# Kernel optimization log

Measured on AMD Instinct MI355X. Metric: run time of the kernel, lower is better.

Reference implementation:

```python
import jax, jax.numpy as jnp
import numpy as np

N, T, J, NB = 2048, 81, 16, 15
D_ATT, HEADS, SEQ, D_LIN, NOISE = 48, 6, 31, 256, 45
BN_EPS, LN_EPS, SLOPE = 1e-5, 1e-6, 0.01

# Human3.6M 16-joint skeleton bone (parent, child) pairs
_BONES = [(0,1),(1,2),(2,3),(0,4),(4,5),(5,6),(0,7),(7,8),(8,9),(9,10),(8,11),(11,12),(12,13),(8,14),(14,15)]
BONES_P = np.array([p for p, c in _BONES])
BONES_C = np.array([c for p, c in _BONES])
_parent = {c: p for p, c in _BONES}
_bone_of = {c: i for i, (p, c) in enumerate(_BONES)}
_M = np.zeros((NB, J), np.float32)  # M[i,j]=1 iff bone i lies on root->joint j chain
for j in range(1, J):
    jj = j
    while jj != 0:
        _M[_bone_of[jj], j] = 1.0
        jj = _parent[jj]
M_BONE2POSE = jnp.asarray(_M)
FIXED_MASK = jnp.ones((NB,), jnp.float32).at[jnp.array([6, 7])].set(0.0)  # torso bones kept fixed


def _layer_norm(t, a, b):
    mean = t.mean(-1, keepdims=True)
    # torch.std default is unbiased (ddof=1); module divides by (std + eps)
    std = jnp.sqrt(((t - mean) ** 2).sum(-1, keepdims=True) / (t.shape[-1] - 1))
    return a * (t - mean) / (std + LN_EPS) + b


def _leaky(x):
    return jnp.where(x >= 0, x, SLOPE * x)


def _axis_angle_to_matrix(v):
    # Rodrigues: v (..., 3) axis-angle -> (..., 3, 3)
    theta = jnp.linalg.norm(v, axis=-1, keepdims=True)
    k = v / jnp.maximum(theta, 1e-8)
    c = jnp.cos(theta)[..., None]
    s = jnp.sin(theta)[..., None]
    kx, ky, kz = k[..., 0], k[..., 1], k[..., 2]
    z = jnp.zeros_like(kx)
    K = jnp.stack([jnp.stack([z, -kz, ky], -1),
                   jnp.stack([kz, z, -kx], -1),
                   jnp.stack([-ky, kx, z], -1)], -2)
    kk = k[..., :, None] * k[..., None, :]
    return c * jnp.eye(3, dtype=v.dtype) + s * K + (1 - c) * kk


def setup_inputs() -> dict:
    key = jax.random.key(0)
    ks = jax.random.split(key, 12)
    w = lambda k, shape, scale=0.05: jax.random.normal(k, shape, jnp.float32) * scale
    return {
        'inputs_3d': jax.random.normal(ks[0], (N, 1, T, J, 3), jnp.float32),
        'noise': jax.random.normal(ks[1], (N, NOISE), jnp.float32),
        'enc_w': w(ks[2], (D_ATT, 3)), 'enc_b': jnp.zeros((D_ATT,), jnp.float32),
        'enc_bn_g': jnp.ones((D_ATT,), jnp.float32), 'enc_bn_b': jnp.zeros((D_ATT,), jnp.float32),
        'ln_a': jnp.ones((D_ATT,), jnp.float32), 'ln_b': jnp.zeros((D_ATT,), jnp.float32),
        'wq': w(ks[3], (D_ATT, D_ATT)), 'bq': jnp.zeros((D_ATT,), jnp.float32),
        'wk': w(ks[4], (D_ATT, D_ATT)), 'bk': jnp.zeros((D_ATT,), jnp.float32),
        'wv': w(ks[5], (D_ATT, D_ATT)), 'bv': jnp.zeros((D_ATT,), jnp.float32),
        'wo': w(ks[6], (D_ATT, D_ATT)), 'bo': jnp.zeros((D_ATT,), jnp.float32),
        'w1': w(ks[7], (D_LIN, SEQ * D_ATT)), 'b1': jnp.zeros((D_LIN,), jnp.float32),
        'bn1_g': jnp.ones((D_LIN,), jnp.float32), 'bn1_b': jnp.zeros((D_LIN,), jnp.float32),
        'w2': w(ks[8], (NB * 4, D_LIN)), 'b2': w(ks[9], (NB * 4,), 0.1),
    }


def reference(inputs_3d, noise, enc_w, enc_b, enc_bn_g, enc_bn_b, ln_a, ln_b,
              wq, bq, wk, bk, wv, bv, wo, bo, w1, b1, bn1_g, bn1_b, w2, b2):
    x5 = inputs_3d[:, 0]                                  # (n, T, 16, 3)
    root = x5[:, :, :1, :]
    x = x5 - root                                         # root-centered
    bvec = x[..., BONES_C, :] - x[..., BONES_P, :]        # (n, T, 15, 3)
    blen = jnp.linalg.norm(bvec, axis=-1, keepdims=True)
    bunit = bvec / blen
    n, t_len = x.shape[0], x.shape[1]
    mid = (t_len - 1) // 2

    x_ = x[:, mid].reshape(n, -1)                         # (n, 48)
    y = jnp.concatenate([x_, noise], axis=-1).reshape(n, SEQ, 3)
    # Conv1d(k=1) == per-token linear; BatchNorm eval (running mean 0, var 1); Dropout off
    y = jax.nn.relu((y @ enc_w.T + enc_b) * enc_bn_g / jnp.sqrt(1.0 + BN_EPS) + enc_bn_b)

    # tiny 6-head self-attention with pre-LayerNorm and residual
    h = _layer_norm(y, ln_a, ln_b)
    d = D_ATT // HEADS
    q = (h @ wq.T + bq).reshape(n, SEQ, HEADS, d).transpose(0, 2, 1, 3)
    k = (h @ wk.T + bk).reshape(n, SEQ, HEADS, d).transpose(0, 2, 1, 3)
    v = (h @ wv.T + bv).reshape(n, SEQ, HEADS, d).transpose(0, 2, 1, 3)
    probs = jax.nn.softmax(jnp.einsum('nhqd,nhkd->nhqk', q, k) / (d ** 0.5), axis=-1)
    ctx = jnp.einsum('nhqk,nhkd->nhqd', probs, v).transpose(0, 2, 1, 3).reshape(n, SEQ, D_ATT)
    y = y + (ctx @ wo.T + bo)

    y = y.reshape(n, -1)                                  # (n, 1488)
    y = _leaky((y @ w1.T + b1) * bn1_g / jnp.sqrt(1.0 + BN_EPS) + bn1_b)
    y = _leaky(y @ w2.T + b2).reshape(n, NB, 4)           # (n, 15, 4)

    axis = y[..., :3]
    axis = axis / jnp.linalg.norm(axis, axis=-1, keepdims=True)
    theta = y[..., 3:4] / t_len                           # (n, 15, 1)
    t_idx = jnp.arange(t_len, dtype=y.dtype)              # (T,)
    vaa = axis[:, None] * (theta[:, None] * t_idx[None, :, None, None])  # (n, T, 15, 3)
    R = _axis_angle_to_matrix(vaa)                        # (n, T, 15, 3, 3)
    mod_unit = jnp.einsum('ntbij,ntbj->ntbi', R, bunit)
    mask = FIXED_MASK[None, None, :, None]
    mod_unit = mod_unit * mask + bunit * (1 - mask)
    ba_diff = 1 - jnp.sum(mod_unit * bunit, axis=-1)      # (n, T, 15)
    mod_bone = mod_unit * blen
    out = jnp.einsum('ntbc,bj->ntjc', mod_bone, M_BONE2POSE) + root  # (n, T, 16, 3)
    return out, ba_diff
```

## Files before the change

### kernel.cpp

```cpp
#include <hip/hip_runtime.h>
#include <math.h>

#define NS   2048
#define TL   81
#define NBN  15
#define DA   48
#define SQL  31
#define KD   1488
#define DL   256
#define MID  40

#define INV_SQRT_BN 0.99999500003749969f
#define SCALE_ATT   0.35355339059327373f

__global__ __launch_bounds__(256)
void attn_kernel(const float* __restrict__ x5, const float* __restrict__ noise,
                 const float* __restrict__ enc_w, const float* __restrict__ enc_b,
                 const float* __restrict__ enc_g, const float* __restrict__ enc_bb,
                 const float* __restrict__ ln_a, const float* __restrict__ ln_b,
                 const float* __restrict__ wq, const float* __restrict__ bq,
                 const float* __restrict__ wk, const float* __restrict__ bk,
                 const float* __restrict__ wv, const float* __restrict__ bv,
                 const float* __restrict__ wo, const float* __restrict__ bo,
                 float* __restrict__ y2)
{
    __shared__ float s93[96];
    __shared__ float sy[32*49];
    __shared__ float sh[32*49];
    __shared__ float sW[3*48*49];
    __shared__ __align__(16) float sQKV[32*148];
    __shared__ float smean[32], sinv[32];

    const int tid = threadIdx.x;
    const int n = blockIdx.x;

    if (tid < 93) {
        float v;
        if (tid < 48) {
            const float* base = x5 + ((size_t)n*TL + MID)*48;
            v = base[tid] - base[tid % 3];
        } else {
            v = noise[(size_t)n*45 + (tid-48)];
        }
        s93[tid] = v;
    }
    #pragma unroll
    for (int l=0; l<9; l++){
        int idx = tid + l*256;
        int f = idx/48, c = idx - f*48;
        int o = f*49 + c;
        sW[o]        = wq[idx];
        sW[2352 + o] = wk[idx];
        sW[4704 + o] = wv[idx];
    }
    __syncthreads();

    for (int idx=tid; idx<SQL*DA; idx+=256){
        int s = idx/48, f = idx - s*48;
        float a = enc_b[f]
                + s93[s*3+0]*enc_w[f*3+0]
                + s93[s*3+1]*enc_w[f*3+1]
                + s93[s*3+2]*enc_w[f*3+2];
        float v = a * (enc_g[f]*INV_SQRT_BN) + enc_bb[f];
        sy[s*49+f] = fmaxf(v, 0.0f);
    }
    __syncthreads();

    if (tid < SQL){
        float m = 0.f;
        for (int f=0; f<48; f++) m += sy[tid*49+f];
        m *= (1.0f/48.0f);
        float vs = 0.f;
        for (int f=0; f<48; f++){ float d = sy[tid*49+f]-m; vs += d*d; }
        float sd = sqrtf(vs * (1.0f/47.0f));
        smean[tid] = m;
        sinv[tid]  = 1.0f/(sd + 1e-6f);
    }
    __syncthreads();

    for (int idx=tid; idx<SQL*DA; idx+=256){
        int s = idx/48, f = idx - s*48;
        sh[s*49+f] = ln_a[f]*(sy[s*49+f]-smean[s])*sinv[s] + ln_b[f];
    }
    __syncthreads();

    if (tid < 192){
        const int sg = tid/24, fg = tid - (tid/24)*24;
        const int arr = fg >> 3;
        const int f0  = (fg & 7)*6;
        const float* wb = sW + arr*2352 + f0*49;
        const float* hb = sh + sg*4*49;
        float a0[6]={0,0,0,0,0,0}, a1[6]={0,0,0,0,0,0};
        float a2[6]={0,0,0,0,0,0}, a3[6]={0,0,0,0,0,0};
        for (int c=0; c<48; c++){
            float h0 = hb[c], h1 = hb[49+c], h2 = hb[98+c], h3 = hb[147+c];
            #pragma unroll
            for (int i=0;i<6;i++){
                float w = wb[i*49+c];
                a0[i] += h0*w; a1[i] += h1*w; a2[i] += h2*w; a3[i] += h3*w;
            }
        }
        const float* bias = (arr==0)? bq : (arr==1? bk : bv);
        #pragma unroll
        for (int i=0;i<6;i++){
            float b = bias[f0+i];
            int col = arr*48 + f0 + i;
            sQKV[(sg*4+0)*148 + col] = a0[i] + b;
            sQKV[(sg*4+1)*148 + col] = a1[i] + b;
            sQKV[(sg*4+2)*148 + col] = a2[i] + b;
            sQKV[(sg*4+3)*148 + col] = a3[i] + b;
        }
    }
    __syncthreads();

    #pragma unroll
    for (int l=0; l<9; l++){
        int idx = tid + l*256;
        sW[(idx/48)*49 + (idx%48)] = wo[idx];
    }
    if (tid < 186){
        const int hd = tid/31, qi = tid - (tid/31)*31;
        const float4 q0 = *(const float4*)(sQKV + qi*148 + hd*8);
        const float4 q1 = *(const float4*)(sQKV + qi*148 + hd*8 + 4);
        float sc[31]; float mx = -1e30f;
        for (int ki=0; ki<31; ki++){
            const float4 k0 = *(const float4*)(sQKV + ki*148 + 48 + hd*8);
            const float4 k1 = *(const float4*)(sQKV + ki*148 + 48 + hd*8 + 4);
            float d = q0.x*k0.x + q0.y*k0.y + q0.z*k0.z + q0.w*k0.w
                    + q1.x*k1.x + q1.y*k1.y + q1.z*k1.z + q1.w*k1.w;
            d *= SCALE_ATT;
            sc[ki] = d; mx = fmaxf(mx, d);
        }
        float ssum = 0.f;
        for (int ki=0; ki<31; ki++){ float e = expf(sc[ki]-mx); sc[ki]=e; ssum += e; }
        float rin = 1.0f/ssum;
        float4 c0 = {0,0,0,0}, c1 = {0,0,0,0};
        for (int ki=0; ki<31; ki++){
            float p = sc[ki];
            const float4 v0 = *(const float4*)(sQKV + ki*148 + 96 + hd*8);
            const float4 v1 = *(const float4*)(sQKV + ki*148 + 96 + hd*8 + 4);
            c0.x += p*v0.x; c0.y += p*v0.y; c0.z += p*v0.z; c0.w += p*v0.w;
            c1.x += p*v1.x; c1.y += p*v1.y; c1.z += p*v1.z; c1.w += p*v1.w;
        }
        float* cb = sh + qi*49 + hd*8;
        cb[0]=c0.x*rin; cb[1]=c0.y*rin; cb[2]=c0.z*rin; cb[3]=c0.w*rin;
        cb[4]=c1.x*rin; cb[5]=c1.y*rin; cb[6]=c1.z*rin; cb[7]=c1.w*rin;
    }
    __syncthreads();

    if (tid < 192){
        const int sg = tid/12, fg = tid - (tid/12)*12;
        const int f0 = fg*4;
        const float* wb = sW + f0*49;
        const float* cb = sh + sg*2*49;
        float a0[4]={0,0,0,0}, a1[4]={0,0,0,0};
        for (int c=0; c<48; c++){
            float x0 = cb[c], x1 = cb[49+c];
            #pragma unroll
            for (int i=0;i<4;i++){
                float w = wb[i*49+c];
                a0[i] += x0*w; a1[i] += x1*w;
            }
        }
        {
            int s = sg*2;
            if (s < 31){
                float* dst = y2 + (size_t)n*KD + s*48 + f0;
                const float* yb = sy + s*49 + f0;
                #pragma unroll
                for (int i=0;i<4;i++) dst[i] = yb[i] + a0[i] + bo[f0+i];
            }
        }
        {
            int s = sg*2+1;
            if (s < 31){
                float* dst = y2 + (size_t)n*KD + s*48 + f0;
                const float* yb = sy + s*49 + f0;
                #pragma unroll
                for (int i=0;i<4;i++) dst[i] = yb[i] + a1[i] + bo[f0+i];
            }
        }
    }
}

#define KSP 6
#define KPS 248
#define KCH 8

__global__ __launch_bounds__(256)
void gemm1_kernel(const float* __restrict__ y2, const float* __restrict__ w1,
                  float* __restrict__ y3raw, int use_partial)
{
    __shared__ __align__(16) float sB[KCH*256];
    __shared__ __align__(16) float sA[KCH*20];
    const int tid = threadIdx.x;
    const int bx = blockIdx.x;
    const int m0 = (bx & 127) * 16;
    const int split = bx >> 7;
    const int ks0 = split * KPS;
    const int c0 = (tid & 15)*4 + (tid >> 6)*64;
    const int r0 = ((tid >> 4) & 3)*4;

    const int bn = tid >> 1;
    const int bg = (tid & 1)*4;
    const int ar = tid >> 1;
    const int ag = (tid & 1)*4;

    float acc[4][4];
    #pragma unroll
    for (int i=0;i<4;i++)
        #pragma unroll
        for (int j=0;j<4;j++) acc[i][j]=0.f;

    for (int ch=0; ch<31; ch++){
        const int k0 = ks0 + ch*KCH;
        float4 b0v = *(const float4*)(w1 + (size_t)bn*KD        + k0 + bg);
        float4 b1v = *(const float4*)(w1 + (size_t)(bn+128)*KD  + k0 + bg);
        float4 av;
        if (tid < 32) av = *(const float4*)(y2 + (size_t)(m0+ar)*KD + k0 + ag);
        __syncthreads();
        sB[(bg+0)*256 + bn] = b0v.x;  sB[(bg+1)*256 + bn] = b0v.y;
        sB[(bg+2)*256 + bn] = b0v.z;  sB[(bg+3)*256 + bn] = b0v.w;
        sB[(bg+0)*256 + bn+128] = b1v.x;  sB[(bg+1)*256 + bn+128] = b1v.y;
        sB[(bg+2)*256 + bn+128] = b1v.z;  sB[(bg+3)*256 + bn+128] = b1v.w;
        if (tid < 32){
            sA[(ag+0)*20 + ar] = av.x;  sA[(ag+1)*20 + ar] = av.y;
            sA[(ag+2)*20 + ar] = av.z;  sA[(ag+3)*20 + ar] = av.w;
        }
        __syncthreads();
        #pragma unroll
        for (int kk=0; kk<KCH; kk++){
            float4 b = *(const float4*)(sB + kk*256 + c0);
            float4 a = *(const float4*)(sA + kk*20 + r0);
            acc[0][0] += a.x*b.x; acc[0][1] += a.x*b.y; acc[0][2] += a.x*b.z; acc[0][3] += a.x*b.w;
            acc[1][0] += a.y*b.x; acc[1][1] += a.y*b.y; acc[1][2] += a.y*b.z; acc[1][3] += a.y*b.w;
            acc[2][0] += a.z*b.x; acc[2][1] += a.z*b.y; acc[2][2] += a.z*b.z; acc[2][3] += a.z*b.w;
            acc[3][0] += a.w*b.x; acc[3][1] += a.w*b.y; acc[3][2] += a.w*b.z; acc[3][3] += a.w*b.w;
        }
    }

    if (use_partial){
        float* dst = y3raw + (size_t)split*NS*DL;
        #pragma unroll
        for (int i=0;i<4;i++){
            float4 v; v.x=acc[i][0]; v.y=acc[i][1]; v.z=acc[i][2]; v.w=acc[i][3];
            *(float4*)(dst + (size_t)(m0+r0+i)*DL + c0) = v;
        }
    } else {
        #pragma unroll
        for (int i=0;i<4;i++)
            #pragma unroll
            for (int j=0;j<4;j++)
                atomicAdd(y3raw + (size_t)(m0+r0+i)*DL + c0 + j, acc[i][j]);
    }
}

__global__ __launch_bounds__(256)
void head_kernel(const float* __restrict__ y3raw, const float* __restrict__ w2,
                 const float* __restrict__ b2, const float* __restrict__ b1,
                 const float* __restrict__ g1, const float* __restrict__ bb1,
                 float* __restrict__ at, int nsl)
{
    __shared__ float swc[64*60];
    __shared__ __align__(16) float sy3[16*256];
    __shared__ float sy4[16*61];
    const int tid = threadIdx.x;
    const int n0 = blockIdx.x * 16;

    #pragma unroll
    for (int l=0;l<4;l++){
        int idx = tid + l*256;
        int s = idx >> 6, i4 = (idx & 63) << 2;
        const float* src = y3raw + (size_t)(n0+s)*256 + i4;
        float4 v = *(const float4*)(src);
        if (nsl == 6){
            #pragma unroll
            for (int sl=1; sl<6; sl++){
                float4 p = *(const float4*)(src + (size_t)sl*NS*DL);
                v.x += p.x; v.y += p.y; v.z += p.z; v.w += p.w;
            }
        }
        const float4 vb = *(const float4*)(b1 + i4);
        const float4 vg = *(const float4*)(g1 + i4);
        const float4 vs = *(const float4*)(bb1 + i4);
        v.x = (v.x + vb.x)*(vg.x*INV_SQRT_BN) + vs.x;  v.x = v.x>=0.f? v.x : 0.01f*v.x;
        v.y = (v.y + vb.y)*(vg.y*INV_SQRT_BN) + vs.y;  v.y = v.y>=0.f? v.y : 0.01f*v.y;
        v.z = (v.z + vb.z)*(vg.z*INV_SQRT_BN) + vs.z;  v.z = v.z>=0.f? v.z : 0.01f*v.z;
        v.w = (v.w + vb.w)*(vg.w*INV_SQRT_BN) + vs.w;  v.w = v.w>=0.f? v.w : 0.01f*v.w;
        *(float4*)(sy3 + s*256 + i4) = v;
    }

    float acc[4]; int ss[4], mm[4];
    #pragma unroll
    for (int l=0;l<4;l++){
        int uu = tid + l*256;
        ss[l]=0; mm[l]=0; acc[l]=0.f;
        if (uu < 960){ ss[l]=uu/60; mm[l]=uu-ss[l]*60; acc[l]=b2[mm[l]]; }
    }

    for (int ch=0; ch<4; ch++){
        const int i0 = ch*64;
        __syncthreads();
        #pragma unroll
        for (int l=0;l<15;l++){
            int idx = tid + l*256;
            int m = idx >> 6, io = idx & 63;
            swc[io*60 + m] = w2[(size_t)m*256 + i0 + io];
        }
        __syncthreads();
        #pragma unroll
        for (int l=0;l<4;l++){
            int uu = tid + l*256;
            if (uu < 960){
                const float* yy = sy3 + ss[l]*256 + i0;
                float a = acc[l];
                #pragma unroll 8
                for (int io=0; io<64; io++) a += yy[io]*swc[io*60 + mm[l]];
                acc[l] = a;
            }
        }
    }
    __syncthreads();
    #pragma unroll
    for (int l=0;l<4;l++){
        int uu = tid + l*256;
        if (uu < 960){
            float a = acc[l];
            sy4[ss[l]*61 + mm[l]] = a>=0.f? a : 0.01f*a;
        }
    }
    __syncthreads();
    if (tid < 240){
        int s = tid/15, b = tid - s*15;
        const float* y4 = sy4 + s*61 + b*4;
        float ax=y4[0], ay=y4[1], az=y4[2], th=y4[3];
        float nr = sqrtf(ax*ax+ay*ay+az*az);
        float4 o;
        o.x = ax/nr; o.y = ay/nr; o.z = az/nr; o.w = th/81.0f;
        *(float4*)(at + (size_t)(n0+s)*60 + b*4) = o;
    }
}

__global__ __launch_bounds__(256)
void pose_kernel(const float* __restrict__ x5, const float* __restrict__ at,
                 float* __restrict__ out)
{
    const int gid = blockIdx.x*256 + threadIdx.x;
    if (gid >= NS*TL) return;
    const int n = gid / TL;
    const int t = gid - n*TL;
    const float ft = (float)t;

    float4 pv[12];
    {
        const float4* src = (const float4*)(x5 + (size_t)gid*48);
        #pragma unroll
        for (int i=0;i<12;i++) pv[i] = src[i];
    }
    float* p = (float*)pv;
    const float4* ab = (const float4*)(at + (size_t)n*60);

    float4 posv[12];
    float* pos = (float*)posv;
    pos[0]=p[0]; pos[1]=p[1]; pos[2]=p[2];
    float ba[15];

    const int PJ[15] = {0,1,2,0,4,5,0,7,8,9,8,11,12,8,14};
    const int CJ[15] = {1,2,3,4,5,6,7,8,9,10,11,12,13,14,15};

    #pragma unroll
    for (int b=0;b<15;b++){
        const int pj = PJ[b], cj = CJ[b];
        float bx = p[cj*3+0]-p[pj*3+0];
        float by = p[cj*3+1]-p[pj*3+1];
        float bz = p[cj*3+2]-p[pj*3+2];
        float bl = sqrtf(bx*bx+by*by+bz*bz);
        float ux = bx/bl, uy = by/bl, uz = bz/bl;
        float mx, my, mz;
        if (b==6 || b==7){
            mx=ux; my=uy; mz=uz;
        } else {
            float4 a = ab[b];
            float ang = a.w * ft;
            float cs = cosf(ang), sn = sinf(ang);
            float kd = a.x*ux + a.y*uy + a.z*uz;
            float cx = a.y*uz - a.z*uy;
            float cy = a.z*ux - a.x*uz;
            float cz = a.x*uy - a.y*ux;
            float oc = (1.0f-cs)*kd;
            mx = ux*cs + cx*sn + a.x*oc;
            my = uy*cs + cy*sn + a.y*oc;
            mz = uz*cs + cz*sn + a.z*oc;
        }
        ba[b] = 1.0f - (mx*ux+my*uy+mz*uz);
        pos[cj*3+0] = pos[pj*3+0] + mx*bl;
        pos[cj*3+1] = pos[pj*3+1] + my*bl;
        pos[cj*3+2] = pos[pj*3+2] + mz*bl;
    }

    {
        float4* dst = (float4*)(out + (size_t)gid*48);
        #pragma unroll
        for (int i=0;i<12;i++) dst[i] = posv[i];
    }
    {
        float* bd = out + (size_t)NS*TL*48 + (size_t)gid*15;
        #pragma unroll
        for (int b=0;b<15;b++) bd[b] = ba[b];
    }
}

extern "C" void kernel_launch(void* const* d_in, const int* in_sizes, int n_in,
                              void* d_out, int out_size, void* d_ws, size_t ws_size,
                              hipStream_t stream)
{
    const float* x5    = (const float*)d_in[0];
    const float* noise = (const float*)d_in[1];
    const float* enc_w = (const float*)d_in[2];
    const float* enc_b = (const float*)d_in[3];
    const float* enc_g = (const float*)d_in[4];
    const float* enc_bb= (const float*)d_in[5];
    const float* ln_a  = (const float*)d_in[6];
    const float* ln_b  = (const float*)d_in[7];
    const float* wq = (const float*)d_in[8];
    const float* bq = (const float*)d_in[9];
    const float* wk = (const float*)d_in[10];
    const float* bk = (const float*)d_in[11];
    const float* wv = (const float*)d_in[12];
    const float* bv = (const float*)d_in[13];
    const float* wo = (const float*)d_in[14];
    const float* bo = (const float*)d_in[15];
    const float* w1 = (const float*)d_in[16];
    const float* b1 = (const float*)d_in[17];
    const float* g1 = (const float*)d_in[18];
    const float* bb1= (const float*)d_in[19];
    const float* w2 = (const float*)d_in[20];
    const float* b2 = (const float*)d_in[21];
    float* out = (float*)d_out;

    float* ws = (float*)d_ws;
    float* y2 = ws;
    float* y3 = y2 + (size_t)NS*KD;

    const size_t need_partial = ((size_t)NS*KD + 6*(size_t)NS*DL + (size_t)NS*60) * 4;
    const int use_partial = (ws_size >= need_partial) ? 1 : 0;
    const int nsl = use_partial ? 6 : 1;
    float* at = y3 + (size_t)nsl*NS*DL;

    if (!use_partial)
        hipMemsetAsync(y3, 0, (size_t)NS*DL*sizeof(float), stream);

    attn_kernel<<<NS, 256, 0, stream>>>(x5, noise, enc_w, enc_b, enc_g, enc_bb,
                                        ln_a, ln_b, wq,bq,wk,bk,wv,bv,wo,bo, y2);
    gemm1_kernel<<<128*KSP, 256, 0, stream>>>(y2, w1, y3, use_partial);
    head_kernel<<<128, 256, 0, stream>>>(y3, w2, b2, b1, g1, bb1, at, nsl);
    pose_kernel<<<(NS*TL+255)/256, 256, 0, stream>>>(x5, at, out);

    (void)in_sizes; (void)n_in; (void)out_size;
}
```

Measured before the change: 250.8 us.

## Widen attention blocks to 512 threads, halve head tile, use fast trig

The attention kernel moves to 512 threads per block, so each thread computes fewer QKV and output-projection rows (2 instead of 4, and 1 instead of 2). The head kernel processes 8 samples per block instead of 16, doubling its grid to 256 blocks to fill more CUs. The pose kernel switches to the __sinf/__cosf intrinsics. Together these aim to raise parallelism in under-occupied kernels and cut trig cost, at the price of less weight reuse per thread, more redundant weight staging in head_kernel, and reduced trig accuracy.

```diff
diff --git a/kernel.cpp b/kernel.cpp
--- a/kernel.cpp
+++ b/kernel.cpp
@@ -13,7 +13,7 @@
 #define INV_SQRT_BN 0.99999500003749969f
 #define SCALE_ATT   0.35355339059327373f
 
-__global__ __launch_bounds__(256)
+__global__ __launch_bounds__(512)
 void attn_kernel(const float* __restrict__ x5, const float* __restrict__ noise,
                  const float* __restrict__ enc_w, const float* __restrict__ enc_b,
                  const float* __restrict__ enc_g, const float* __restrict__ enc_bb,
@@ -45,17 +45,19 @@
         s93[tid] = v;
     }
     #pragma unroll
-    for (int l=0; l<9; l++){
-        int idx = tid + l*256;
-        int f = idx/48, c = idx - f*48;
-        int o = f*49 + c;
-        sW[o]        = wq[idx];
-        sW[2352 + o] = wk[idx];
-        sW[4704 + o] = wv[idx];
-    }
-    __syncthreads();
-
-    for (int idx=tid; idx<SQL*DA; idx+=256){
+    for (int l=0; l<5; l++){
+        int idx = tid + l*512;
+        if (idx < 2304){
+            int f = idx/48, c = idx - f*48;
+            int o = f*49 + c;
+            sW[o]        = wq[idx];
+            sW[2352 + o] = wk[idx];
+            sW[4704 + o] = wv[idx];
+        }
+    }
+    __syncthreads();
+
+    for (int idx=tid; idx<SQL*DA; idx+=512){
         int s = idx/48, f = idx - s*48;
         float a = enc_b[f]
                 + s93[s*3+0]*enc_w[f*3+0]
@@ -78,26 +80,25 @@
     }
     __syncthreads();
 
-    for (int idx=tid; idx<SQL*DA; idx+=256){
+    for (int idx=tid; idx<SQL*DA; idx+=512){
         int s = idx/48, f = idx - s*48;
         sh[s*49+f] = ln_a[f]*(sy[s*49+f]-smean[s])*sinv[s] + ln_b[f];
     }
     __syncthreads();
 
-    if (tid < 192){
+    if (tid < 384){
         const int sg = tid/24, fg = tid - (tid/24)*24;
         const int arr = fg >> 3;
         const int f0  = (fg & 7)*6;
         const float* wb = sW + arr*2352 + f0*49;
-        const float* hb = sh + sg*4*49;
+        const float* hb = sh + sg*2*49;
         float a0[6]={0,0,0,0,0,0}, a1[6]={0,0,0,0,0,0};
-        float a2[6]={0,0,0,0,0,0}, a3[6]={0,0,0,0,0,0};
         for (int c=0; c<48; c++){
-            float h0 = hb[c], h1 = hb[49+c], h2 = hb[98+c], h3 = hb[147+c];
+            float h0 = hb[c], h1 = hb[49+c];
             #pragma unroll
             for (int i=0;i<6;i++){
                 float w = wb[i*49+c];
-                a0[i] += h0*w; a1[i] += h1*w; a2[i] += h2*w; a3[i] += h3*w;
+                a0[i] += h0*w; a1[i] += h1*w;
             }
         }
         const float* bias = (arr==0)? bq : (arr==1? bk : bv);
@@ -105,18 +106,17 @@
         for (int i=0;i<6;i++){
             float b = bias[f0+i];
             int col = arr*48 + f0 + i;
-            sQKV[(sg*4+0)*148 + col] = a0[i] + b;
-            sQKV[(sg*4+1)*148 + col] = a1[i] + b;
-            sQKV[(sg*4+2)*148 + col] = a2[i] + b;
-            sQKV[(sg*4+3)*148 + col] = a3[i] + b;
-        }
-    }
-    __syncthreads();
-
-    #pragma unroll
-    for (int l=0; l<9; l++){
-        int idx = tid + l*256;
-        sW[(idx/48)*49 + (idx%48)] = wo[idx];
+            sQKV[(sg*2+0)*148 + col] = a0[i] + b;
+            sQKV[(sg*2+1)*148 + col] = a1[i] + b;
+        }
+    }
+    __syncthreads();
+
+    #pragma unroll
+    for (int l=0; l<5; l++){
+        int idx = tid + l*512;
+        if (idx < 2304)
+            sW[(idx/48)*49 + (idx%48)] = wo[idx];
     }
     if (tid < 186){
         const int hd = tid/31, qi = tid - (tid/31)*31;
@@ -148,37 +148,25 @@
     }
     __syncthreads();
 
-    if (tid < 192){
+    if (tid < 384){
         const int sg = tid/12, fg = tid - (tid/12)*12;
         const int f0 = fg*4;
-        const float* wb = sW + f0*49;
-        const float* cb = sh + sg*2*49;
-        float a0[4]={0,0,0,0}, a1[4]={0,0,0,0};
-        for (int c=0; c<48; c++){
-            float x0 = cb[c], x1 = cb[49+c];
+        if (sg < 31){
+            const float* wb = sW + f0*49;
+            const float* cb = sh + sg*49;
+            float a0[4]={0,0,0,0};
+            for (int c=0; c<48; c++){
+                float x0 = cb[c];
+                #pragma unroll
+                for (int i=0;i<4;i++){
+                    float w = wb[i*49+c];
+                    a0[i] += x0*w;
+                }
+            }
+            float* dst = y2 + (size_t)n*KD + sg*48 + f0;
+            const float* yb = sy + sg*49 + f0;
             #pragma unroll
-            for (int i=0;i<4;i++){
-                float w = wb[i*49+c];
-                a0[i] += x0*w; a1[i] += x1*w;
-            }
-        }
-        {
-            int s = sg*2;
-            if (s < 31){
-                float* dst = y2 + (size_t)n*KD + s*48 + f0;
-                const float* yb = sy + s*49 + f0;
-                #pragma unroll
-                for (int i=0;i<4;i++) dst[i] = yb[i] + a0[i] + bo[f0+i];
-            }
-        }
-        {
-            int s = sg*2+1;
-            if (s < 31){
-                float* dst = y2 + (size_t)n*KD + s*48 + f0;
-                const float* yb = sy + s*49 + f0;
-                #pragma unroll
-                for (int i=0;i<4;i++) dst[i] = yb[i] + a1[i] + bo[f0+i];
-            }
+            for (int i=0;i<4;i++) dst[i] = yb[i] + a0[i] + bo[f0+i];
         }
     }
 }
@@ -262,13 +250,13 @@
                  float* __restrict__ at, int nsl)
 {
     __shared__ float swc[64*60];
-    __shared__ __align__(16) float sy3[16*256];
-    __shared__ float sy4[16*61];
+    __shared__ __align__(16) float sy3[8*256];
+    __shared__ float sy4[8*61];
     const int tid = threadIdx.x;
-    const int n0 = blockIdx.x * 16;
-
-    #pragma unroll
-    for (int l=0;l<4;l++){
+    const int n0 = blockIdx.x * 8;
+
+    #pragma unroll
+    for (int l=0;l<2;l++){
         int idx = tid + l*256;
         int s = idx >> 6, i4 = (idx & 63) << 2;
         const float* src = y3raw + (size_t)(n0+s)*256 + i4;
@@ -290,12 +278,12 @@
         *(float4*)(sy3 + s*256 + i4) = v;
     }
 
-    float acc[4]; int ss[4], mm[4];
-    #pragma unroll
-    for (int l=0;l<4;l++){
+    float acc[2]; int ss[2], mm[2];
+    #pragma unroll
+    for (int l=0;l<2;l++){
         int uu = tid + l*256;
         ss[l]=0; mm[l]=0; acc[l]=0.f;
-        if (uu < 960){ ss[l]=uu/60; mm[l]=uu-ss[l]*60; acc[l]=b2[mm[l]]; }
+        if (uu < 480){ ss[l]=uu/60; mm[l]=uu-ss[l]*60; acc[l]=b2[mm[l]]; }
     }
 
     for (int ch=0; ch<4; ch++){
@@ -309,9 +297,9 @@
         }
         __syncthreads();
         #pragma unroll
-        for (int l=0;l<4;l++){
+        for (int l=0;l<2;l++){
             int uu = tid + l*256;
-            if (uu < 960){
+            if (uu < 480){
                 const float* yy = sy3 + ss[l]*256 + i0;
                 float a = acc[l];
                 #pragma unroll 8
@@ -322,15 +310,15 @@
     }
     __syncthreads();
     #pragma unroll
-    for (int l=0;l<4;l++){
+    for (int l=0;l<2;l++){
         int uu = tid + l*256;
-        if (uu < 960){
+        if (uu < 480){
             float a = acc[l];
             sy4[ss[l]*61 + mm[l]] = a>=0.f? a : 0.01f*a;
         }
     }
     __syncthreads();
-    if (tid < 240){
+    if (tid < 120){
         int s = tid/15, b = tid - s*15;
         const float* y4 = sy4 + s*61 + b*4;
         float ax=y4[0], ay=y4[1], az=y4[2], th=y4[3];
@@ -382,7 +370,7 @@
         } else {
             float4 a = ab[b];
             float ang = a.w * ft;
-            float cs = cosf(ang), sn = sinf(ang);
+            float cs = __cosf(ang), sn = __sinf(ang);
             float kd = a.x*ux + a.y*uy + a.z*uz;
             float cx = a.y*uz - a.z*uy;
             float cy = a.z*ux - a.x*uz;
@@ -450,10 +438,10 @@
     if (!use_partial)
         hipMemsetAsync(y3, 0, (size_t)NS*DL*sizeof(float), stream);
 
-    attn_kernel<<<NS, 256, 0, stream>>>(x5, noise, enc_w, enc_b, enc_g, enc_bb,
+    attn_kernel<<<NS, 512, 0, stream>>>(x5, noise, enc_w, enc_b, enc_g, enc_bb,
                                         ln_a, ln_b, wq,bq,wk,bk,wv,bv,wo,bo, y2);
     gemm1_kernel<<<128*KSP, 256, 0, stream>>>(y2, w1, y3, use_partial);
-    head_kernel<<<128, 256, 0, stream>>>(y3, w2, b2, b1, g1, bb1, at, nsl);
+    head_kernel<<<NS/8, 256, 0, stream>>>(y3, w2, b2, b1, g1, bb1, at, nsl);
     pose_kernel<<<(NS*TL+255)/256, 256, 0, stream>>>(x5, at, out);
 
     (void)in_sizes; (void)n_in; (void)out_size;
```

Result: slower. 272.6 us (+8.7%).

## Store split-K partials in output buffer, halve head block size, use fast trig

Applied to the files above, without the earlier changes.

The split-K partial sums of the first GEMM now always go to the output buffer as scratch, which is large enough and is overwritten later by the pose kernel. This removes the atomicAdd fallback and the memset. The head kernel now handles 8 samples per block instead of 16, giving 256 blocks rather than 128 for better occupancy across CUs. The pose kernel switches to the __sinf/__cosf intrinsics, which lowers accuracy in exchange for cheaper trig.

```diff
diff --git a/kernel.cpp b/kernel.cpp
--- a/kernel.cpp
+++ b/kernel.cpp
@@ -189,7 +189,7 @@
 
 __global__ __launch_bounds__(256)
 void gemm1_kernel(const float* __restrict__ y2, const float* __restrict__ w1,
-                  float* __restrict__ y3raw, int use_partial)
+                  float* __restrict__ y3p)
 {
     __shared__ __align__(16) float sB[KCH*256];
     __shared__ __align__(16) float sA[KCH*20];
@@ -239,46 +239,36 @@
         }
     }
 
-    if (use_partial){
-        float* dst = y3raw + (size_t)split*NS*DL;
-        #pragma unroll
-        for (int i=0;i<4;i++){
-            float4 v; v.x=acc[i][0]; v.y=acc[i][1]; v.z=acc[i][2]; v.w=acc[i][3];
-            *(float4*)(dst + (size_t)(m0+r0+i)*DL + c0) = v;
-        }
-    } else {
-        #pragma unroll
-        for (int i=0;i<4;i++)
-            #pragma unroll
-            for (int j=0;j<4;j++)
-                atomicAdd(y3raw + (size_t)(m0+r0+i)*DL + c0 + j, acc[i][j]);
+    float* dst = y3p + (size_t)split*NS*DL;
+    #pragma unroll
+    for (int i=0;i<4;i++){
+        float4 v; v.x=acc[i][0]; v.y=acc[i][1]; v.z=acc[i][2]; v.w=acc[i][3];
+        *(float4*)(dst + (size_t)(m0+r0+i)*DL + c0) = v;
     }
 }
 
 __global__ __launch_bounds__(256)
-void head_kernel(const float* __restrict__ y3raw, const float* __restrict__ w2,
+void head_kernel(const float* __restrict__ y3p, const float* __restrict__ w2,
                  const float* __restrict__ b2, const float* __restrict__ b1,
                  const float* __restrict__ g1, const float* __restrict__ bb1,
-                 float* __restrict__ at, int nsl)
+                 float* __restrict__ at)
 {
     __shared__ float swc[64*60];
-    __shared__ __align__(16) float sy3[16*256];
-    __shared__ float sy4[16*61];
+    __shared__ __align__(16) float sy3[8*256];
+    __shared__ float sy4[8*61];
     const int tid = threadIdx.x;
-    const int n0 = blockIdx.x * 16;
-
-    #pragma unroll
-    for (int l=0;l<4;l++){
+    const int n0 = blockIdx.x * 8;
+
+    #pragma unroll
+    for (int l=0;l<2;l++){
         int idx = tid + l*256;
         int s = idx >> 6, i4 = (idx & 63) << 2;
-        const float* src = y3raw + (size_t)(n0+s)*256 + i4;
+        const float* src = y3p + (size_t)(n0+s)*256 + i4;
         float4 v = *(const float4*)(src);
-        if (nsl == 6){
-            #pragma unroll
-            for (int sl=1; sl<6; sl++){
-                float4 p = *(const float4*)(src + (size_t)sl*NS*DL);
-                v.x += p.x; v.y += p.y; v.z += p.z; v.w += p.w;
-            }
+        #pragma unroll
+        for (int sl=1; sl<6; sl++){
+            float4 p = *(const float4*)(src + (size_t)sl*NS*DL);
+            v.x += p.x; v.y += p.y; v.z += p.z; v.w += p.w;
         }
         const float4 vb = *(const float4*)(b1 + i4);
         const float4 vg = *(const float4*)(g1 + i4);
@@ -290,12 +280,12 @@
         *(float4*)(sy3 + s*256 + i4) = v;
     }
 
-    float acc[4]; int ss[4], mm[4];
-    #pragma unroll
-    for (int l=0;l<4;l++){
+    float acc[2]; int ss[2], mm[2];
+    #pragma unroll
+    for (int l=0;l<2;l++){
         int uu = tid + l*256;
         ss[l]=0; mm[l]=0; acc[l]=0.f;
-        if (uu < 960){ ss[l]=uu/60; mm[l]=uu-ss[l]*60; acc[l]=b2[mm[l]]; }
+        if (uu < 480){ ss[l]=uu/60; mm[l]=uu-ss[l]*60; acc[l]=b2[mm[l]]; }
     }
 
     for (int ch=0; ch<4; ch++){
@@ -309,9 +299,9 @@
         }
         __syncthreads();
         #pragma unroll
-        for (int l=0;l<4;l++){
+        for (int l=0;l<2;l++){
             int uu = tid + l*256;
-            if (uu < 960){
+            if (uu < 480){
                 const float* yy = sy3 + ss[l]*256 + i0;
                 float a = acc[l];
                 #pragma unroll 8
@@ -322,15 +312,15 @@
     }
     __syncthreads();
     #pragma unroll
-    for (int l=0;l<4;l++){
+    for (int l=0;l<2;l++){
         int uu = tid + l*256;
-        if (uu < 960){
+        if (uu < 480){
             float a = acc[l];
             sy4[ss[l]*61 + mm[l]] = a>=0.f? a : 0.01f*a;
         }
     }
     __syncthreads();
-    if (tid < 240){
+    if (tid < 120){
         int s = tid/15, b = tid - s*15;
         const float* y4 = sy4 + s*61 + b*4;
         float ax=y4[0], ay=y4[1], az=y4[2], th=y4[3];
@@ -382,7 +372,7 @@
         } else {
             float4 a = ab[b];
             float ang = a.w * ft;
-            float cs = cosf(ang), sn = sinf(ang);
+            float cs = __cosf(ang), sn = __sinf(ang);
             float kd = a.x*ux + a.y*uy + a.z*uz;
             float cx = a.y*uz - a.z*uy;
             float cy = a.z*ux - a.x*uz;
@@ -440,21 +430,15 @@
 
     float* ws = (float*)d_ws;
     float* y2 = ws;
-    float* y3 = y2 + (size_t)NS*KD;
-
-    const size_t need_partial = ((size_t)NS*KD + 6*(size_t)NS*DL + (size_t)NS*60) * 4;
-    const int use_partial = (ws_size >= need_partial) ? 1 : 0;
-    const int nsl = use_partial ? 6 : 1;
-    float* at = y3 + (size_t)nsl*NS*DL;
-
-    if (!use_partial)
-        hipMemsetAsync(y3, 0, (size_t)NS*DL*sizeof(float), stream);
+    float* at = y2 + (size_t)NS*KD;
+
+    float* y3p = out;
 
     attn_kernel<<<NS, 256, 0, stream>>>(x5, noise, enc_w, enc_b, enc_g, enc_bb,
                                         ln_a, ln_b, wq,bq,wk,bk,wv,bv,wo,bo, y2);
-    gemm1_kernel<<<128*KSP, 256, 0, stream>>>(y2, w1, y3, use_partial);
-    head_kernel<<<128, 256, 0, stream>>>(y3, w2, b2, b1, g1, bb1, at, nsl);
+    gemm1_kernel<<<128*KSP, 256, 0, stream>>>(y2, w1, y3p);
+    head_kernel<<<NS/8, 256, 0, stream>>>(y3p, w2, b2, b1, g1, bb1, at);
     pose_kernel<<<(NS*TL+255)/256, 256, 0, stream>>>(x5, at, out);
 
-    (void)in_sizes; (void)n_in; (void)out_size;
+    (void)in_sizes; (void)n_in; (void)out_size; (void)ws_size;
 }
```

Measured after the change: 237.5 us. 5.3% less time.
